# Optimization experiments

Hardware: AMD Instinct MI355X
Metric: run time of the kernel (lower is better)

The kernel has to match this reference:

```python
import jax, jax.numpy as jnp
import numpy as np

KERNEL = 5
PAD = (KERNEL - 1) // 2  # fixed_padding with dilation=1: pad_beg = pad_end = 2


def setup_inputs() -> dict:
    key = jax.random.key(0)
    kx, kw = jax.random.split(key)
    x = jax.random.normal(kx, (4, 4, 1024, 1024), dtype=jnp.float32)
    weight = jax.random.normal(kw, (4, 4, KERNEL, KERNEL), dtype=jnp.float32)
    return {"x": x, "weight": weight}


def reference(x, weight):
    """Morphological dilation2d: out[b,o,h,w] = max_{c,i,j} (x_pad[b,c,h+i,w+j] + w[o,c,i,j]).

    Equivalent to the torch unfold + broadcast-add + max over dim C*k*k, but computed
    as a fused sliding-window max-plus without materializing the im2col tensor.
    """
    B, C, H, W = x.shape
    k = weight.shape[-1]
    xp = jnp.pad(x, ((0, 0), (0, 0), (PAD, PAD), (PAD, PAD)))  # zero pad, same as F.pad
    out = None
    for i in range(k):
        for j in range(k):
            patch = xp[:, :, i:i + H, j:j + W]          # (B, C, H, W)
            w_ij = weight[:, :, i, j]                    # (O, C)
            # max over in_channels of (x + w) for this tap
            val = jnp.max(patch[:, None] + w_ij[None, :, :, None, None], axis=2)  # (B, O, H, W)
            out = val if out is None else jnp.maximum(out, val)
    return out
```

## Files before the change

kernel.cpp:

```cpp
#include <hip/hip_runtime.h>


constexpr int Himg = 1024, Wimg = 1024, Cin = 4, Cout = 4, Kn = 5;
constexpr int TH = 8, TW = 128;
constexpr int LR = TH + 4;
constexpr int LC = TW + 8;
constexpr int LC4 = LC / 4;

typedef float v2f __attribute__((ext_vector_type(2)));

__global__ void reorg_w(const float* __restrict__ w, float* __restrict__ wt) {
  int idx = threadIdx.x;
  if (idx < Cout * Cin * Kn * Kn) {
    int o  = idx / (Cin * Kn * Kn);
    int r  = idx % (Cin * Kn * Kn);
    int c  = r / (Kn * Kn);
    int r2 = r % (Kn * Kn);
    int i  = r2 / Kn, j = r2 % Kn;
    wt[((c * Kn + i) * Kn + j) * Cout + o] = w[idx];
  }
}

__device__ __forceinline__ float max5(float a, float b, float c, float d, float e) {
  return fmaxf(fmaxf(a, b), fmaxf(c, fmaxf(d, e)));
}

template <bool TRANS>
__global__ __launch_bounds__(256) void morph(const float* __restrict__ x,
                                             const float* __restrict__ wt,
                                             float* __restrict__ out) {
  __shared__ __align__(16) float xs[Cin][LR][LC];
  const int tid = threadIdx.x;
  const int tile_w0 = blockIdx.x * TW;
  const int tile_r0 = blockIdx.y * TH;
  const int b = blockIdx.z;

  for (int idx = tid; idx < Cin * LR * LC4; idx += 256) {
    const int c   = idx / (LR * LC4);
    const int rem = idx - c * (LR * LC4);
    const int row = rem / LC4;
    const int ch  = rem - row * LC4;
    const int gr  = tile_r0 - 2 + row;
    const int gc  = tile_w0 - 4 + ch * 4;
    float4 v = make_float4(0.f, 0.f, 0.f, 0.f);
    if ((unsigned)gr < (unsigned)Himg) {
      const float* src = x + ((size_t)(b * Cin + c) * Himg + gr) * Wimg;
      if (gc >= 0 && gc <= Wimg - 4) {
        v = *(const float4*)(src + gc);
      } else {
        if ((unsigned)(gc + 0) < (unsigned)Wimg) v.x = src[gc + 0];
        if ((unsigned)(gc + 1) < (unsigned)Wimg) v.y = src[gc + 1];
        if ((unsigned)(gc + 2) < (unsigned)Wimg) v.z = src[gc + 2];
        if ((unsigned)(gc + 3) < (unsigned)Wimg) v.w = src[gc + 3];
      }
    }
    *(float4*)&xs[c][row][ch * 4] = v;
  }
  __syncthreads();

  const int tx = tid & 31;
  const int ty = tid >> 5;

  float acc[Cout][4];
#pragma unroll
  for (int o = 0; o < Cout; ++o)
#pragma unroll
    for (int p = 0; p < 4; ++p) acc[o][p] = -3.4e38f;

#define ACC_O(O, WA)                                                                     \
  do {                                                                                   \
    v2f p01[5], p23[5];                                                                  \
    _Pragma("unroll") for (int j = 0; j < 5; ++j) {                                      \
      v2f wb = {WA[j], WA[j]};                                                           \
      v2f a2 = {win[2 + j], win[3 + j]};                                                 \
      v2f b2 = {win[4 + j], win[5 + j]};                                                 \
      p01[j] = a2 + wb;                                                                  \
      p23[j] = b2 + wb;                                                                  \
    }                                                                                    \
    acc[O][0] = fmaxf(acc[O][0], max5(p01[0].x, p01[1].x, p01[2].x, p01[3].x, p01[4].x)); \
    acc[O][1] = fmaxf(acc[O][1], max5(p01[0].y, p01[1].y, p01[2].y, p01[3].y, p01[4].y)); \
    acc[O][2] = fmaxf(acc[O][2], max5(p23[0].x, p23[1].x, p23[2].x, p23[3].x, p23[4].x)); \
    acc[O][3] = fmaxf(acc[O][3], max5(p23[0].y, p23[1].y, p23[2].y, p23[3].y, p23[4].y)); \
  } while (0)

#pragma unroll 1
  for (int c = 0; c < Cin; ++c) {
#pragma unroll
    for (int i = 0; i < Kn; ++i) {
      const float* rowp = &xs[c][ty + i][tx * 4];
      float4 q0 = *(const float4*)(rowp);
      float4 q1 = *(const float4*)(rowp + 4);
      float4 q2 = *(const float4*)(rowp + 8);
      float win[12] = {q0.x, q0.y, q0.z, q0.w, q1.x, q1.y, q1.z, q1.w,
                       q2.x, q2.y, q2.z, q2.w};

      float wo0[5], wo1[5], wo2[5], wo3[5];
      if (TRANS) {
        const float4* wq = (const float4*)wt + (c * Kn + i) * Kn;
#pragma unroll
        for (int j = 0; j < Kn; ++j) {
          float4 wv = wq[j];
          wo0[j] = wv.x; wo1[j] = wv.y; wo2[j] = wv.z; wo3[j] = wv.w;
        }
      } else {
#pragma unroll
        for (int j = 0; j < Kn; ++j) {
          wo0[j] = wt[((0 * Cin + c) * Kn + i) * Kn + j];
          wo1[j] = wt[((1 * Cin + c) * Kn + i) * Kn + j];
          wo2[j] = wt[((2 * Cin + c) * Kn + i) * Kn + j];
          wo3[j] = wt[((3 * Cin + c) * Kn + i) * Kn + j];
        }
      }

      ACC_O(0, wo0);
      ACC_O(1, wo1);
      ACC_O(2, wo2);
      ACC_O(3, wo3);
    }
  }
#undef ACC_O

  const int r = tile_r0 + ty;
  const int gc0 = tile_w0 + tx * 4;
#pragma unroll
  for (int o = 0; o < Cout; ++o) {
    float4 res = make_float4(acc[o][0], acc[o][1], acc[o][2], acc[o][3]);
    *(float4*)&out[((size_t)(b * Cout + o) * Himg + r) * Wimg + gc0] = res;
  }
}

extern "C" void kernel_launch(void* const* d_in, const int* in_sizes, int n_in,
                              void* d_out, int out_size, void* d_ws, size_t ws_size,
                              hipStream_t stream) {
  const float* x = (const float*)d_in[0];
  const float* w = (const float*)d_in[1];
  float* out = (float*)d_out;

  dim3 grid(Wimg / TW, Himg / TH, 4);

  if (ws_size >= sizeof(float) * Cout * Cin * Kn * Kn) {
    float* wt = (float*)d_ws;
    reorg_w<<<dim3(1), dim3(512), 0, stream>>>(w, wt);
    morph<true><<<grid, dim3(256), 0, stream>>>(x, wt, out);
  } else {
    morph<false><<<grid, dim3(256), 0, stream>>>(x, w, out);
  }
}
```

Before: 155.2 us.

## Pack output-channel pairs into v_pk_add_f32 with op_sel and stage weights in LDS

Drops the separate weight-reorg kernel launch and instead has every block transpose the weights into shared memory. The inner loop now pairs two output channels per packed register and uses inline-asm v_pk_add_f32 with op_sel to broadcast one input pixel across both lanes. This is meant to halve the scalar add count and remove the broadcast moves. It adds per-block weight staging, and the inline asm may limit compiler scheduling.

```diff
diff --git a/kernel.cpp b/kernel.cpp
--- a/kernel.cpp
+++ b/kernel.cpp
@@ -6,34 +6,42 @@
 constexpr int LR = TH + 4;
 constexpr int LC = TW + 8;
 constexpr int LC4 = LC / 4;
+constexpr int NW = Cout * Cin * Kn * Kn;
 
 typedef float v2f __attribute__((ext_vector_type(2)));
 
-__global__ void reorg_w(const float* __restrict__ w, float* __restrict__ wt) {
-  int idx = threadIdx.x;
-  if (idx < Cout * Cin * Kn * Kn) {
-    int o  = idx / (Cin * Kn * Kn);
-    int r  = idx % (Cin * Kn * Kn);
-    int c  = r / (Kn * Kn);
-    int r2 = r % (Kn * Kn);
-    int i  = r2 / Kn, j = r2 % Kn;
-    wt[((c * Kn + i) * Kn + j) * Cout + o] = w[idx];
-  }
+__device__ __forceinline__ v2f pk_add_lo(v2f xp, v2f wp) {
+  v2f d;
+  asm("v_pk_add_f32 %0, %1, %2 op_sel:[0,0] op_sel_hi:[0,1]"
+      : "=v"(d) : "v"(xp), "v"(wp));
+  return d;
+}
+__device__ __forceinline__ v2f pk_add_hi(v2f xp, v2f wp) {
+  v2f d;
+  asm("v_pk_add_f32 %0, %1, %2 op_sel:[1,0] op_sel_hi:[1,1]"
+      : "=v"(d) : "v"(xp), "v"(wp));
+  return d;
 }
 
-__device__ __forceinline__ float max5(float a, float b, float c, float d, float e) {
-  return fmaxf(fmaxf(a, b), fmaxf(c, fmaxf(d, e)));
-}
-
-template <bool TRANS>
 __global__ __launch_bounds__(256) void morph(const float* __restrict__ x,
-                                             const float* __restrict__ wt,
+                                             const float* __restrict__ w,
                                              float* __restrict__ out) {
   __shared__ __align__(16) float xs[Cin][LR][LC];
+  __shared__ __align__(16) float ws[Cin][Kn][Kn][Cout];
+
   const int tid = threadIdx.x;
   const int tile_w0 = blockIdx.x * TW;
   const int tile_r0 = blockIdx.y * TH;
   const int b = blockIdx.z;
+
+  for (int t = tid; t < NW; t += 256) {
+    const int o  = t / (Cin * Kn * Kn);
+    const int r  = t % (Cin * Kn * Kn);
+    const int c  = r / (Kn * Kn);
+    const int r2 = r % (Kn * Kn);
+    const int i  = r2 / Kn, j = r2 % Kn;
+    ws[c][i][j][o] = w[t];
+  }
 
   for (int idx = tid; idx < Cin * LR * LC4; idx += 256) {
     const int c   = idx / (LR * LC4);
@@ -61,71 +69,70 @@
   const int tx = tid & 31;
   const int ty = tid >> 5;
 
-  float acc[Cout][4];
+  v2f a01[4], a23[4];
 #pragma unroll
-  for (int o = 0; o < Cout; ++o)
-#pragma unroll
-    for (int p = 0; p < 4; ++p) acc[o][p] = -3.4e38f;
-
-#define ACC_O(O, WA)                                                                     \
-  do {                                                                                   \
-    v2f p01[5], p23[5];                                                                  \
-    _Pragma("unroll") for (int j = 0; j < 5; ++j) {                                      \
-      v2f wb = {WA[j], WA[j]};                                                           \
-      v2f a2 = {win[2 + j], win[3 + j]};                                                 \
-      v2f b2 = {win[4 + j], win[5 + j]};                                                 \
-      p01[j] = a2 + wb;                                                                  \
-      p23[j] = b2 + wb;                                                                  \
-    }                                                                                    \
-    acc[O][0] = fmaxf(acc[O][0], max5(p01[0].x, p01[1].x, p01[2].x, p01[3].x, p01[4].x)); \
-    acc[O][1] = fmaxf(acc[O][1], max5(p01[0].y, p01[1].y, p01[2].y, p01[3].y, p01[4].y)); \
-    acc[O][2] = fmaxf(acc[O][2], max5(p23[0].x, p23[1].x, p23[2].x, p23[3].x, p23[4].x)); \
-    acc[O][3] = fmaxf(acc[O][3], max5(p23[0].y, p23[1].y, p23[2].y, p23[3].y, p23[4].y)); \
-  } while (0)
+  for (int p = 0; p < 4; ++p) {
+    a01[p].x = -3.4e38f; a01[p].y = -3.4e38f;
+    a23[p].x = -3.4e38f; a23[p].y = -3.4e38f;
+  }
 
 #pragma unroll 1
   for (int c = 0; c < Cin; ++c) {
 #pragma unroll
     for (int i = 0; i < Kn; ++i) {
       const float* rowp = &xs[c][ty + i][tx * 4];
-      float4 q0 = *(const float4*)(rowp);
-      float4 q1 = *(const float4*)(rowp + 4);
-      float4 q2 = *(const float4*)(rowp + 8);
-      float win[12] = {q0.x, q0.y, q0.z, q0.w, q1.x, q1.y, q1.z, q1.w,
-                       q2.x, q2.y, q2.z, q2.w};
+      v2f P[5];
+      P[1] = *(const v2f*)(rowp + 2);
+      P[2] = *(const v2f*)(rowp + 4);
+      P[3] = *(const v2f*)(rowp + 6);
+      P[4] = *(const v2f*)(rowp + 8);
 
-      float wo0[5], wo1[5], wo2[5], wo3[5];
-      if (TRANS) {
-        const float4* wq = (const float4*)wt + (c * Kn + i) * Kn;
+      const v2f* wp = (const v2f*)&ws[c][i][0][0];
+      v2f w01[5], w23[5];
+#pragma unroll
+      for (int j = 0; j < Kn; ++j) {
+        w01[j] = wp[2 * j];
+        w23[j] = wp[2 * j + 1];
+      }
+
+#pragma unroll
+      for (int p = 0; p < 4; ++p) {
+        v2f q01[5], q23[5];
 #pragma unroll
         for (int j = 0; j < Kn; ++j) {
-          float4 wv = wq[j];
-          wo0[j] = wv.x; wo1[j] = wv.y; wo2[j] = wv.z; wo3[j] = wv.w;
+          const int idx = 2 + p + j;
+          const v2f xp = P[idx >> 1];
+          if (idx & 1) {
+            q01[j] = pk_add_hi(xp, w01[j]);
+            q23[j] = pk_add_hi(xp, w23[j]);
+          } else {
+            q01[j] = pk_add_lo(xp, w01[j]);
+            q23[j] = pk_add_lo(xp, w23[j]);
+          }
         }
-      } else {
-#pragma unroll
-        for (int j = 0; j < Kn; ++j) {
-          wo0[j] = wt[((0 * Cin + c) * Kn + i) * Kn + j];
-          wo1[j] = wt[((1 * Cin + c) * Kn + i) * Kn + j];
-          wo2[j] = wt[((2 * Cin + c) * Kn + i) * Kn + j];
-          wo3[j] = wt[((3 * Cin + c) * Kn + i) * Kn + j];
-        }
+        a01[p].x = fmaxf(fmaxf(fmaxf(q01[0].x, q01[1].x), q01[2].x),
+                         fmaxf(fmaxf(q01[3].x, q01[4].x), a01[p].x));
+        a01[p].y = fmaxf(fmaxf(fmaxf(q01[0].y, q01[1].y), q01[2].y),
+                         fmaxf(fmaxf(q01[3].y, q01[4].y), a01[p].y));
+        a23[p].x = fmaxf(fmaxf(fmaxf(q23[0].x, q23[1].x), q23[2].x),
+                         fmaxf(fmaxf(q23[3].x, q23[4].x), a23[p].x));
+        a23[p].y = fmaxf(fmaxf(fmaxf(q23[0].y, q23[1].y), q23[2].y),
+                         fmaxf(fmaxf(q23[3].y, q23[4].y), a23[p].y));
       }
-
-      ACC_O(0, wo0);
-      ACC_O(1, wo1);
-      ACC_O(2, wo2);
-      ACC_O(3, wo3);
     }
   }
-#undef ACC_O
 
   const int r = tile_r0 + ty;
   const int gc0 = tile_w0 + tx * 4;
-#pragma unroll
-  for (int o = 0; o < Cout; ++o) {
-    float4 res = make_float4(acc[o][0], acc[o][1], acc[o][2], acc[o][3]);
-    *(float4*)&out[((size_t)(b * Cout + o) * Himg + r) * Wimg + gc0] = res;
+  {
+    float4 r0 = make_float4(a01[0].x, a01[1].x, a01[2].x, a01[3].x);
+    float4 r1 = make_float4(a01[0].y, a01[1].y, a01[2].y, a01[3].y);
+    float4 r2 = make_float4(a23[0].x, a23[1].x, a23[2].x, a23[3].x);
+    float4 r3 = make_float4(a23[0].y, a23[1].y, a23[2].y, a23[3].y);
+    *(float4*)&out[((size_t)(b * Cout + 0) * Himg + r) * Wimg + gc0] = r0;
+    *(float4*)&out[((size_t)(b * Cout + 1) * Himg + r) * Wimg + gc0] = r1;
+    *(float4*)&out[((size_t)(b * Cout + 2) * Himg + r) * Wimg + gc0] = r2;
+    *(float4*)&out[((size_t)(b * Cout + 3) * Himg + r) * Wimg + gc0] = r3;
   }
 }
 
@@ -137,12 +144,5 @@
   float* out = (float*)d_out;
 
   dim3 grid(Wimg / TW, Himg / TH, 4);
-
-  if (ws_size >= sizeof(float) * Cout * Cin * Kn * Kn) {
-    float* wt = (float*)d_ws;
-    reorg_w<<<dim3(1), dim3(512), 0, stream>>>(w, wt);
-    morph<true><<<grid, dim3(256), 0, stream>>>(x, wt, out);
-  } else {
-    morph<false><<<grid, dim3(256), 0, stream>>>(x, w, out);
-  }
+  morph<<<grid, dim3(256), 0, stream>>>(x, w, out);
 }
```

New measurement: 172.0 us. 1.11x slower.
